# Performance work log

Hardware: AMD Instinct MI355X
Metric: run time of the kernel (lower is better)

The kernel has to match this reference:

```python
import jax, jax.numpy as jnp
import numpy as np

N_NODES = 100000
N_EDGES = 500000
IN_DIM, HID, N_CLS = 128, 512, 40


def gcn_conv(x, W, b, src, dst, num_nodes):
    # PyG GCNConv: h = x W; add self-loops; norm = d^-1/2[src] * d^-1/2[dst];
    # out[dst] += norm * h[src]; out += bias
    h = x @ W  # [N, out_dim]
    ones = jnp.ones(src.shape[0], dtype=x.dtype)
    deg = jax.ops.segment_sum(ones, dst, num_segments=num_nodes)  # in-degree incl self-loops
    dinv = jnp.where(deg > 0, jax.lax.rsqrt(deg), 0.0)
    norm = dinv[src] * dinv[dst]  # [E]
    msgs = h[src] * norm[:, None]  # [E, out_dim] gather + scale
    out = jax.ops.segment_sum(msgs, dst, num_segments=num_nodes)
    return out + b


def setup_inputs() -> dict:
    key = jax.random.key(0)
    k1, k2, k3, k4, k5, k6 = jax.random.split(key, 6)
    x = jax.random.normal(k1, (N_NODES, IN_DIM), dtype=jnp.float32)
    edge_index = jax.random.randint(k2, (2, N_EDGES), 0, N_NODES, dtype=jnp.int32)
    # Glorot-ish params
    W1 = jax.random.normal(k3, (IN_DIM, HID), dtype=jnp.float32) * (1.0 / np.sqrt(IN_DIM))
    b1 = jnp.zeros((HID,), dtype=jnp.float32)
    W2 = jax.random.normal(k4, (HID, N_CLS), dtype=jnp.float32) * (1.0 / np.sqrt(HID))
    b2 = jnp.zeros((N_CLS,), dtype=jnp.float32)
    return {"x": x, "edge_index": edge_index, "W1": W1, "b1": b1, "W2": W2, "b2": b2}


def reference(x, edge_index, W1, b1, W2, b2):
    n = x.shape[0]
    # add self-loops once, shared by both conv layers
    loop = jnp.arange(n, dtype=edge_index.dtype)
    src = jnp.concatenate([edge_index[0], loop])
    dst = jnp.concatenate([edge_index[1], loop])
    h = gcn_conv(x, W1, b1, src, dst, n)
    h = jax.nn.relu(h)
    # dropout is identity in eval mode (reference computed in eval)
    h = gcn_conv(h, W2, b2, src, dst, n)
    return jax.nn.log_softmax(h, axis=1)
```

## Files before the change

kernel.cpp:

```cpp
#include <hip/hip_runtime.h>
#include <cstdint>
#include <cstddef>

#define N_NODES 100000
#define N_EDGES 500000
#define IN_DIM  128
#define HID     512
#define N_CLS   40
#define N_SBLK  ((N_NODES + 255) / 256)
#define N_CNTB  ((N_EDGES + 255) / 256)
#define N_XBFB  12500
#define N_PREPB 352

typedef short bf16x8 __attribute__((ext_vector_type(8)));
typedef float f32x4 __attribute__((ext_vector_type(4)));

__device__ inline unsigned short f2bf(float f) {
  unsigned u = __float_as_uint(f);
  u = u + 0x7fffu + ((u >> 16) & 1u);
  return (unsigned short)(u >> 16);
}
__device__ inline float blo(unsigned u) { return __uint_as_float(u << 16); }
__device__ inline float bhi(unsigned u) { return __uint_as_float(u & 0xffff0000u); }

__global__ __launch_bounds__(256) void k_zero(int* __restrict__ cnt, unsigned* __restrict__ flags) {
  int i = blockIdx.x * 256 + threadIdx.x;
  if (i < N_NODES) cnt[i] = 0;
  if (i < 512) flags[i] = 0;
}

__global__ __launch_bounds__(256) void k_count_xbf(const int* __restrict__ dst, int* __restrict__ cnt,
                                                   const float* __restrict__ x, uint2* __restrict__ xb2) {
  int b = blockIdx.x;
  if (b < N_CNTB) {
    int e = b * 256 + threadIdx.x;
    if (e < N_EDGES) atomicAdd(&cnt[dst[e]], 1);
  } else {
    int t = (b - N_CNTB) * 256 + threadIdx.x;
    float4 v = ((const float4*)x)[t];
    uint2 o;
    o.x = (unsigned)f2bf(v.x) | ((unsigned)f2bf(v.y) << 16);
    o.y = (unsigned)f2bf(v.z) | ((unsigned)f2bf(v.w) << 16);
    xb2[t] = o;
  }
}

__global__ __launch_bounds__(256) void k_scan_prep(const int* __restrict__ cnt, unsigned* __restrict__ flags,
                                                   int* __restrict__ offsets, int* __restrict__ cursor,
                                                   float* __restrict__ dinv,
                                                   const float* __restrict__ W1, const float* __restrict__ W2,
                                                   unsigned short* __restrict__ W1F, unsigned short* __restrict__ W2F) {
  int b = blockIdx.x;
  if (b < N_SBLK) {
    __shared__ int s[256];
    __shared__ int base_sh;
    int i = b * 256 + threadIdx.x;
    int v = (i < N_NODES) ? cnt[i] : 0;
    s[threadIdx.x] = v;
    __syncthreads();
    #pragma unroll
    for (int off = 1; off < 256; off <<= 1) {
      int t = (threadIdx.x >= off) ? s[threadIdx.x - off] : 0;
      __syncthreads();
      s[threadIdx.x] += t;
      __syncthreads();
    }
    int incl = s[threadIdx.x];
    if (threadIdx.x == 0) {
      int total = s[255];
      if (b == 0) {
        atomicExch(&flags[0], (2u << 30) | (unsigned)total);
        base_sh = 0;
      } else {
        atomicExch(&flags[b], (1u << 30) | (unsigned)total);
        int base = 0, pred = b - 1;
        while (true) {
          unsigned f;
          do { f = atomicAdd(&flags[pred], 0u); } while ((f >> 30) == 0u);
          base += (int)(f & 0x3fffffffu);
          if ((f >> 30) == 2u) break;
          --pred;
        }
        atomicExch(&flags[b], (2u << 30) | (unsigned)(base + (unsigned)total));
        base_sh = base;
      }
    }
    __syncthreads();
    int gbase = base_sh;
    if (i < N_NODES) {
      int excl = gbase + incl - v;
      offsets[i] = excl;
      cursor[i]  = excl;
      dinv[i]    = rsqrtf((float)(v + 1));
    }
    if (b == 0 && threadIdx.x == 0) offsets[N_NODES] = N_EDGES;
  } else {
    int t = (b - N_SBLK) * 256 + threadIdx.x;
    if (t < 65536) {
      int j = t & 7, lane = (t >> 3) & 63, rest = t >> 9;
      int s2 = rest & 3, c = rest >> 2;
      int k = s2 * 32 + (lane >> 4) * 8 + j;
      int n = c * 16 + (lane & 15);
      W1F[t] = f2bf(W1[k * HID + n]);
    } else {
      int u = t - 65536;
      int j = u & 7, lane = (u >> 3) & 63, rest = u >> 9;
      int ct = rest % 3, gk = rest / 3;
      int k = gk * 32 + (lane >> 4) * 8 + j;
      int col = ct * 16 + (lane & 15);
      W2F[u] = (col < N_CLS) ? f2bf(W2[k * N_CLS + col]) : (unsigned short)0;
    }
  }
}

__global__ __launch_bounds__(256) void k_fill(const int* __restrict__ src, const int* __restrict__ dst,
                                              const float* __restrict__ dinv,
                                              int* __restrict__ cursor, int2* __restrict__ epair) {
  int e = blockIdx.x * 256 + threadIdx.x;
  if (e >= N_EDGES) return;
  int s = src[e], d = dst[e];
  int pos = atomicAdd(&cursor[d], 1);
  float nrm = dinv[s] * dinv[d];
  epair[pos] = make_int2(s, __float_as_int(nrm));
}

__global__ __launch_bounds__(256) void k_gather1(const uint2* __restrict__ xb, const int2* __restrict__ ep,
                                                 const int* __restrict__ offsets,
                                                 const float* __restrict__ dinv, uint2* __restrict__ z1) {
  int lane = threadIdx.x & 63, h = lane >> 5, l = lane & 31;
  int d = blockIdx.x * 8 + (threadIdx.x >> 6) * 2 + h;
  int start = offsets[d], end = offsets[d + 1];
  float dd = dinv[d], sl = dd * dd;
  uint2 su = xb[(size_t)d * 32 + l];
  float a0 = sl * blo(su.x), a1 = sl * bhi(su.x), a2 = sl * blo(su.y), a3 = sl * bhi(su.y);
  float p0a = 0.f, p1a = 0.f, p2a = 0.f, p3a = 0.f;
  float q0a = 0.f, q1a = 0.f, q2a = 0.f, q3a = 0.f;
  float r0a = 0.f, r1a = 0.f, r2a = 0.f, r3a = 0.f;

  int i = start;
  for (; i + 3 < end; i += 4) {
    int2 e0 = ep[i], e1 = ep[i + 1], e2 = ep[i + 2], e3 = ep[i + 3];
    uint2 r0 = xb[(size_t)e0.x * 32 + l];
    uint2 r1 = xb[(size_t)e1.x * 32 + l];
    uint2 r2 = xb[(size_t)e2.x * 32 + l];
    uint2 r3 = xb[(size_t)e3.x * 32 + l];
    float n0 = __int_as_float(e0.y), n1 = __int_as_float(e1.y);
    float n2 = __int_as_float(e2.y), n3 = __int_as_float(e3.y);
    a0  += n0 * blo(r0.x); a1  += n0 * bhi(r0.x); a2  += n0 * blo(r0.y); a3  += n0 * bhi(r0.y);
    p0a += n1 * blo(r1.x); p1a += n1 * bhi(r1.x); p2a += n1 * blo(r1.y); p3a += n1 * bhi(r1.y);
    q0a += n2 * blo(r2.x); q1a += n2 * bhi(r2.x); q2a += n2 * blo(r2.y); q3a += n2 * bhi(r2.y);
    r0a += n3 * blo(r3.x); r1a += n3 * bhi(r3.x); r2a += n3 * blo(r3.y); r3a += n3 * bhi(r3.y);
  }
  for (; i < end; ++i) {
    int2 e0 = ep[i];
    uint2 r0 = xb[(size_t)e0.x * 32 + l];
    float n0 = __int_as_float(e0.y);
    a0 += n0 * blo(r0.x); a1 += n0 * bhi(r0.x); a2 += n0 * blo(r0.y); a3 += n0 * bhi(r0.y);
  }
  a0 += p0a + q0a + r0a;
  a1 += p1a + q1a + r1a;
  a2 += p2a + q2a + r2a;
  a3 += p3a + q3a + r3a;
  uint2 o;
  o.x = (unsigned)f2bf(a0) | ((unsigned)f2bf(a1) << 16);
  o.y = (unsigned)f2bf(a2) | ((unsigned)f2bf(a3) << 16);
  z1[(size_t)d * 32 + l] = o;
}

#define HS_STRIDE 56
__global__ __launch_bounds__(256) void k_fused_mfma(const unsigned short* __restrict__ z1b,
                                                    const unsigned short* __restrict__ W1F,
                                                    const float* __restrict__ b1,
                                                    const unsigned short* __restrict__ W2F,
                                                    unsigned short* __restrict__ Pb) {
  __shared__ unsigned short Hs[4][64 * HS_STRIDE];
  const int tid  = threadIdx.x;
  const int w    = tid >> 6, lane = tid & 63;
  const int c16  = lane & 15, quad = lane >> 4;
  const int mbase = blockIdx.x * 256 + w * 64;

  bf16x8 afrag[4][4];
  #pragma unroll
  for (int t = 0; t < 4; ++t) {
    int mrow = mbase + t * 16 + c16;
    int meff = (mrow < N_NODES) ? mrow : 0;
    const bf16x8* arow = (const bf16x8*)(z1b + (size_t)meff * IN_DIM + quad * 8);
    afrag[t][0] = arow[0];
    afrag[t][1] = arow[4];
    afrag[t][2] = arow[8];
    afrag[t][3] = arow[12];
  }

  f32x4 pacc[4][3];
  #pragma unroll
  for (int t = 0; t < 4; ++t)
    #pragma unroll
    for (int ct = 0; ct < 3; ++ct) pacc[t][ct] = (f32x4){0.f, 0.f, 0.f, 0.f};

  const bf16x8* w1f = (const bf16x8*)W1F;
  const bf16x8* w2f = (const bf16x8*)W2F;
  unsigned short* hs = Hs[w];

  for (int g = 0; g < 16; ++g) {
    #pragma unroll
    for (int nt = 0; nt < 2; ++nt) {
      int c = g * 2 + nt;
      bf16x8 bp0 = w1f[(c * 4 + 0) * 64 + lane];
      bf16x8 bp1 = w1f[(c * 4 + 1) * 64 + lane];
      bf16x8 bp2 = w1f[(c * 4 + 2) * 64 + lane];
      bf16x8 bp3 = w1f[(c * 4 + 3) * 64 + lane];
      f32x4 h[4];
      #pragma unroll
      for (int t = 0; t < 4; ++t) h[t] = (f32x4){0.f, 0.f, 0.f, 0.f};
      #pragma unroll
      for (int t = 0; t < 4; ++t) h[t] = __builtin_amdgcn_mfma_f32_16x16x32_bf16(afrag[t][0], bp0, h[t], 0, 0, 0);
      #pragma unroll
      for (int t = 0; t < 4; ++t) h[t] = __builtin_amdgcn_mfma_f32_16x16x32_bf16(afrag[t][1], bp1, h[t], 0, 0, 0);
      #pragma unroll
      for (int t = 0; t < 4; ++t) h[t] = __builtin_amdgcn_mfma_f32_16x16x32_bf16(afrag[t][2], bp2, h[t], 0, 0, 0);
      #pragma unroll
      for (int t = 0; t < 4; ++t) h[t] = __builtin_amdgcn_mfma_f32_16x16x32_bf16(afrag[t][3], bp3, h[t], 0, 0, 0);
      float bias = b1[c * 16 + c16];
      #pragma unroll
      for (int t = 0; t < 4; ++t)
        #pragma unroll
        for (int r = 0; r < 4; ++r)
          hs[(t * 16 + quad * 4 + r) * HS_STRIDE + nt * 16 + c16] = f2bf(fmaxf(h[t][r] + bias, 0.f));
    }
    bf16x8 hf[4];
    #pragma unroll
    for (int t = 0; t < 4; ++t)
      hf[t] = *(const bf16x8*)(hs + (t * 16 + c16) * HS_STRIDE + quad * 8);
    #pragma unroll
    for (int ct = 0; ct < 3; ++ct) {
      bf16x8 bf = w2f[(g * 3 + ct) * 64 + lane];
      #pragma unroll
      for (int t = 0; t < 4; ++t)
        pacc[t][ct] = __builtin_amdgcn_mfma_f32_16x16x32_bf16(hf[t], bf, pacc[t][ct], 0, 0, 0);
    }
  }

  #pragma unroll
  for (int t = 0; t < 4; ++t) {
    int mrow0 = mbase + t * 16 + quad * 4;
    #pragma unroll
    for (int ct = 0; ct < 3; ++ct) {
      int col = ct * 16 + c16;
      if (col < N_CLS) {
        #pragma unroll
        for (int r = 0; r < 4; ++r) {
          int m = mrow0 + r;
          if (m < N_NODES) Pb[(size_t)m * N_CLS + col] = f2bf(pacc[t][ct][r]);
        }
      }
    }
  }
}

__global__ __launch_bounds__(256) void k_gather2_lsm(const uint2* __restrict__ Pu2,
                                                     const int2* __restrict__ ep,
                                                     const int* __restrict__ offsets,
                                                     const float* __restrict__ dinv, const float* __restrict__ b2,
                                                     float* __restrict__ out) {
  int lane = threadIdx.x & 63, q = lane >> 4, l = lane & 15;
  int d = blockIdx.x * 16 + (threadIdx.x >> 6) * 4 + q;
  bool act = l < 10;
  int lc = act ? l : 0;
  int start = offsets[d], end = offsets[d + 1];
  float dd = dinv[d], sl = dd * dd;

  uint2 su = Pu2[(size_t)d * 10 + lc];
  float a0 = sl * blo(su.x), a1 = sl * bhi(su.x), a2 = sl * blo(su.y), a3 = sl * bhi(su.y);
  float p0a = 0.f, p1a = 0.f, p2a = 0.f, p3a = 0.f;
  float q0a = 0.f, q1a = 0.f, q2a = 0.f, q3a = 0.f;
  float r0a = 0.f, r1a = 0.f, r2a = 0.f, r3a = 0.f;

  int i = start;
  for (; i + 3 < end; i += 4) {
    int2 e0 = ep[i], e1 = ep[i + 1], e2 = ep[i + 2], e3 = ep[i + 3];
    uint2 u0 = Pu2[(size_t)e0.x * 10 + lc];
    uint2 u1 = Pu2[(size_t)e1.x * 10 + lc];
    uint2 u2 = Pu2[(size_t)e2.x * 10 + lc];
    uint2 u3 = Pu2[(size_t)e3.x * 10 + lc];
    float n0 = __int_as_float(e0.y), n1 = __int_as_float(e1.y);
    float n2 = __int_as_float(e2.y), n3 = __int_as_float(e3.y);
    a0  += n0 * blo(u0.x); a1  += n0 * bhi(u0.x); a2  += n0 * blo(u0.y); a3  += n0 * bhi(u0.y);
    p0a += n1 * blo(u1.x); p1a += n1 * bhi(u1.x); p2a += n1 * blo(u1.y); p3a += n1 * bhi(u1.y);
    q0a += n2 * blo(u2.x); q1a += n2 * bhi(u2.x); q2a += n2 * blo(u2.y); q3a += n2 * bhi(u2.y);
    r0a += n3 * blo(u3.x); r1a += n3 * bhi(u3.x); r2a += n3 * blo(u3.y); r3a += n3 * bhi(u3.y);
  }
  for (; i < end; ++i) {
    int2 e0 = ep[i];
    uint2 u0 = Pu2[(size_t)e0.x * 10 + lc];
    float n0 = __int_as_float(e0.y);
    a0 += n0 * blo(u0.x); a1 += n0 * bhi(u0.x); a2 += n0 * blo(u0.y); a3 += n0 * bhi(u0.y);
  }

  float v0, v1, v2, v3;
  if (act) {
    float4 bb = ((const float4*)b2)[l];
    v0 = a0 + p0a + q0a + r0a + bb.x;
    v1 = a1 + p1a + q1a + r1a + bb.y;
    v2 = a2 + p2a + q2a + r2a + bb.z;
    v3 = a3 + p3a + q3a + r3a + bb.w;
  } else {
    v0 = v1 = v2 = v3 = -1e30f;
  }
  float m = fmaxf(fmaxf(v0, v1), fmaxf(v2, v3));
  #pragma unroll
  for (int off = 8; off > 0; off >>= 1) m = fmaxf(m, __shfl_xor(m, off, 64));
  float e = act ? (expf(v0 - m) + expf(v1 - m) + expf(v2 - m) + expf(v3 - m)) : 0.f;
  float s = e;
  #pragma unroll
  for (int off = 8; off > 0; off >>= 1) s += __shfl_xor(s, off, 64);
  float lse = m + logf(s);
  if (act) {
    float4 o = make_float4(v0 - lse, v1 - lse, v2 - lse, v3 - lse);
    ((float4*)(out + (size_t)d * N_CLS))[l] = o;
  }
}

extern "C" void kernel_launch(void* const* d_in, const int* in_sizes, int n_in,
                              void* d_out, int out_size, void* d_ws, size_t ws_size,
                              hipStream_t stream) {
  const float* x  = (const float*)d_in[0];
  const int*   ei = (const int*)d_in[1];
  const int*  src = ei;
  const int*  dst = ei + N_EDGES;
  const float* W1 = (const float*)d_in[2];
  const float* b1 = (const float*)d_in[3];
  const float* W2 = (const float*)d_in[4];
  const float* b2 = (const float*)d_in[5];
  float* out = (float*)d_out;

  float* dinv    = (float*)d_ws;
  int*   cnt     = (int*)(dinv + 131072);
  int*   offsets = cnt + 131072;
  int*   cursor  = offsets + 131072;
  unsigned* flags = (unsigned*)(cursor + 131072);
  int2*  epair   = (int2*)(flags + 1024);
  uint2* xb2     = (uint2*)(epair + 524288);
  unsigned short* Pb = (unsigned short*)xb2;
  unsigned short* z1b = (unsigned short*)(xb2 + 3200000);
  unsigned short* W1F = z1b + (size_t)N_NODES * IN_DIM;
  unsigned short* W2F = W1F + HID * IN_DIM;

  k_zero <<<(N_NODES + 255) / 256, 256, 0, stream>>>(cnt, flags);
  k_count_xbf<<<N_CNTB + N_XBFB, 256, 0, stream>>>(dst, cnt, x, xb2);
  k_scan_prep<<<N_SBLK + N_PREPB, 256, 0, stream>>>(cnt, flags, offsets, cursor, dinv, W1, W2, W1F, W2F);
  k_fill <<<N_CNTB, 256, 0, stream>>>(src, dst, dinv, cursor, epair);
  k_gather1<<<N_NODES / 8, 256, 0, stream>>>(xb2, epair, offsets, dinv, (uint2*)z1b);
  k_fused_mfma<<<(N_NODES + 255) / 256, 256, 0, stream>>>(z1b, W1F, b1, W2F, Pb);
  k_gather2_lsm<<<N_NODES / 16, 256, 0, stream>>>((const uint2*)Pb, epair, offsets, dinv, b2, out);
}
```

Baseline: 247.4 us.

## Use nontemporal loads/stores, predicated 8-wide gather loops, and memset zeroing

Replaces the custom zero kernel with two hipMemsetAsync calls. Adds nontemporal stores for the bf16 x copy, z1, P and the final output, and nontemporal loads for the edge pairs. Rewrites both gather loops as 8-wide predicated batches, with invalid slots clamped to index 0 and weight 0, and two accumulator sets instead of four plus a tail loop. This aims to keep more gathers in flight and reduce cache pollution from streaming data. In exchange it issues wasted loads for short neighbor lists and reads epair past end, and nontemporal stores of data that is read back soon may lose cache reuse.

```diff
diff --git a/kernel.cpp b/kernel.cpp
--- a/kernel.cpp
+++ b/kernel.cpp
@@ -14,6 +14,8 @@
 
 typedef short bf16x8 __attribute__((ext_vector_type(8)));
 typedef float f32x4 __attribute__((ext_vector_type(4)));
+typedef int   i32x2 __attribute__((ext_vector_type(2)));
+typedef unsigned u32x2 __attribute__((ext_vector_type(2)));
 
 __device__ inline unsigned short f2bf(float f) {
   unsigned u = __float_as_uint(f);
@@ -23,14 +25,8 @@
 __device__ inline float blo(unsigned u) { return __uint_as_float(u << 16); }
 __device__ inline float bhi(unsigned u) { return __uint_as_float(u & 0xffff0000u); }
 
-__global__ __launch_bounds__(256) void k_zero(int* __restrict__ cnt, unsigned* __restrict__ flags) {
-  int i = blockIdx.x * 256 + threadIdx.x;
-  if (i < N_NODES) cnt[i] = 0;
-  if (i < 512) flags[i] = 0;
-}
-
 __global__ __launch_bounds__(256) void k_count_xbf(const int* __restrict__ dst, int* __restrict__ cnt,
-                                                   const float* __restrict__ x, uint2* __restrict__ xb2) {
+                                                   const float* __restrict__ x, unsigned* __restrict__ xb) {
   int b = blockIdx.x;
   if (b < N_CNTB) {
     int e = b * 256 + threadIdx.x;
@@ -38,10 +34,10 @@
   } else {
     int t = (b - N_CNTB) * 256 + threadIdx.x;
     float4 v = ((const float4*)x)[t];
-    uint2 o;
+    u32x2 o;
     o.x = (unsigned)f2bf(v.x) | ((unsigned)f2bf(v.y) << 16);
     o.y = (unsigned)f2bf(v.z) | ((unsigned)f2bf(v.w) << 16);
-    xb2[t] = o;
+    __builtin_nontemporal_store(o, (u32x2*)(xb + 2 * (size_t)t));
   }
 }
 
@@ -124,47 +120,35 @@
   epair[pos] = make_int2(s, __float_as_int(nrm));
 }
 
-__global__ __launch_bounds__(256) void k_gather1(const uint2* __restrict__ xb, const int2* __restrict__ ep,
+__global__ __launch_bounds__(256) void k_gather1(const uint2* __restrict__ xb, const i32x2* __restrict__ ep,
                                                  const int* __restrict__ offsets,
-                                                 const float* __restrict__ dinv, uint2* __restrict__ z1) {
+                                                 const float* __restrict__ dinv, unsigned* __restrict__ z1) {
   int lane = threadIdx.x & 63, h = lane >> 5, l = lane & 31;
   int d = blockIdx.x * 8 + (threadIdx.x >> 6) * 2 + h;
   int start = offsets[d], end = offsets[d + 1];
   float dd = dinv[d], sl = dd * dd;
   uint2 su = xb[(size_t)d * 32 + l];
-  float a0 = sl * blo(su.x), a1 = sl * bhi(su.x), a2 = sl * blo(su.y), a3 = sl * bhi(su.y);
-  float p0a = 0.f, p1a = 0.f, p2a = 0.f, p3a = 0.f;
-  float q0a = 0.f, q1a = 0.f, q2a = 0.f, q3a = 0.f;
-  float r0a = 0.f, r1a = 0.f, r2a = 0.f, r3a = 0.f;
-
-  int i = start;
-  for (; i + 3 < end; i += 4) {
-    int2 e0 = ep[i], e1 = ep[i + 1], e2 = ep[i + 2], e3 = ep[i + 3];
-    uint2 r0 = xb[(size_t)e0.x * 32 + l];
-    uint2 r1 = xb[(size_t)e1.x * 32 + l];
-    uint2 r2 = xb[(size_t)e2.x * 32 + l];
-    uint2 r3 = xb[(size_t)e3.x * 32 + l];
-    float n0 = __int_as_float(e0.y), n1 = __int_as_float(e1.y);
-    float n2 = __int_as_float(e2.y), n3 = __int_as_float(e3.y);
-    a0  += n0 * blo(r0.x); a1  += n0 * bhi(r0.x); a2  += n0 * blo(r0.y); a3  += n0 * bhi(r0.y);
-    p0a += n1 * blo(r1.x); p1a += n1 * bhi(r1.x); p2a += n1 * blo(r1.y); p3a += n1 * bhi(r1.y);
-    q0a += n2 * blo(r2.x); q1a += n2 * bhi(r2.x); q2a += n2 * blo(r2.y); q3a += n2 * bhi(r2.y);
-    r0a += n3 * blo(r3.x); r1a += n3 * bhi(r3.x); r2a += n3 * blo(r3.y); r3a += n3 * bhi(r3.y);
-  }
-  for (; i < end; ++i) {
-    int2 e0 = ep[i];
-    uint2 r0 = xb[(size_t)e0.x * 32 + l];
-    float n0 = __int_as_float(e0.y);
-    a0 += n0 * blo(r0.x); a1 += n0 * bhi(r0.x); a2 += n0 * blo(r0.y); a3 += n0 * bhi(r0.y);
-  }
-  a0 += p0a + q0a + r0a;
-  a1 += p1a + q1a + r1a;
-  a2 += p2a + q2a + r2a;
-  a3 += p3a + q3a + r3a;
-  uint2 o;
-  o.x = (unsigned)f2bf(a0) | ((unsigned)f2bf(a1) << 16);
-  o.y = (unsigned)f2bf(a2) | ((unsigned)f2bf(a3) << 16);
-  z1[(size_t)d * 32 + l] = o;
+  float s0 = sl * blo(su.x), s1 = sl * bhi(su.x), s2 = sl * blo(su.y), s3 = sl * bhi(su.y);
+  float t0 = 0.f, t1 = 0.f, t2 = 0.f, t3 = 0.f;
+
+  for (int i = start; i < end; i += 8) {
+    i32x2 e[8];
+    #pragma unroll
+    for (int k = 0; k < 8; ++k) e[k] = __builtin_nontemporal_load(&ep[i + k]);
+    #pragma unroll
+    for (int k = 0; k < 8; ++k) {
+      bool val = (i + k) < end;
+      int idx  = val ? e[k].x : 0;
+      float n  = val ? __int_as_float(e[k].y) : 0.f;
+      uint2 r  = xb[(size_t)idx * 32 + l];
+      if (k & 1) { t0 += n * blo(r.x); t1 += n * bhi(r.x); t2 += n * blo(r.y); t3 += n * bhi(r.y); }
+      else       { s0 += n * blo(r.x); s1 += n * bhi(r.x); s2 += n * blo(r.y); s3 += n * bhi(r.y); }
+    }
+  }
+  u32x2 o;
+  o.x = (unsigned)f2bf(s0 + t0) | ((unsigned)f2bf(s1 + t1) << 16);
+  o.y = (unsigned)f2bf(s2 + t2) | ((unsigned)f2bf(s3 + t3) << 16);
+  __builtin_nontemporal_store(o, (u32x2*)(z1 + 2 * ((size_t)d * 32 + l)));
 }
 
 #define HS_STRIDE 56
@@ -250,7 +234,8 @@
         #pragma unroll
         for (int r = 0; r < 4; ++r) {
           int m = mrow0 + r;
-          if (m < N_NODES) Pb[(size_t)m * N_CLS + col] = f2bf(pacc[t][ct][r]);
+          if (m < N_NODES)
+            __builtin_nontemporal_store(f2bf(pacc[t][ct][r]), &Pb[(size_t)m * N_CLS + col]);
         }
       }
     }
@@ -258,7 +243,7 @@
 }
 
 __global__ __launch_bounds__(256) void k_gather2_lsm(const uint2* __restrict__ Pu2,
-                                                     const int2* __restrict__ ep,
+                                                     const i32x2* __restrict__ ep,
                                                      const int* __restrict__ offsets,
                                                      const float* __restrict__ dinv, const float* __restrict__ b2,
                                                      float* __restrict__ out) {
@@ -270,39 +255,31 @@
   float dd = dinv[d], sl = dd * dd;
 
   uint2 su = Pu2[(size_t)d * 10 + lc];
-  float a0 = sl * blo(su.x), a1 = sl * bhi(su.x), a2 = sl * blo(su.y), a3 = sl * bhi(su.y);
-  float p0a = 0.f, p1a = 0.f, p2a = 0.f, p3a = 0.f;
-  float q0a = 0.f, q1a = 0.f, q2a = 0.f, q3a = 0.f;
-  float r0a = 0.f, r1a = 0.f, r2a = 0.f, r3a = 0.f;
-
-  int i = start;
-  for (; i + 3 < end; i += 4) {
-    int2 e0 = ep[i], e1 = ep[i + 1], e2 = ep[i + 2], e3 = ep[i + 3];
-    uint2 u0 = Pu2[(size_t)e0.x * 10 + lc];
-    uint2 u1 = Pu2[(size_t)e1.x * 10 + lc];
-    uint2 u2 = Pu2[(size_t)e2.x * 10 + lc];
-    uint2 u3 = Pu2[(size_t)e3.x * 10 + lc];
-    float n0 = __int_as_float(e0.y), n1 = __int_as_float(e1.y);
-    float n2 = __int_as_float(e2.y), n3 = __int_as_float(e3.y);
-    a0  += n0 * blo(u0.x); a1  += n0 * bhi(u0.x); a2  += n0 * blo(u0.y); a3  += n0 * bhi(u0.y);
-    p0a += n1 * blo(u1.x); p1a += n1 * bhi(u1.x); p2a += n1 * blo(u1.y); p3a += n1 * bhi(u1.y);
-    q0a += n2 * blo(u2.x); q1a += n2 * bhi(u2.x); q2a += n2 * blo(u2.y); q3a += n2 * bhi(u2.y);
-    r0a += n3 * blo(u3.x); r1a += n3 * bhi(u3.x); r2a += n3 * blo(u3.y); r3a += n3 * bhi(u3.y);
-  }
-  for (; i < end; ++i) {
-    int2 e0 = ep[i];
-    uint2 u0 = Pu2[(size_t)e0.x * 10 + lc];
-    float n0 = __int_as_float(e0.y);
-    a0 += n0 * blo(u0.x); a1 += n0 * bhi(u0.x); a2 += n0 * blo(u0.y); a3 += n0 * bhi(u0.y);
+  float s0 = sl * blo(su.x), s1 = sl * bhi(su.x), s2 = sl * blo(su.y), s3 = sl * bhi(su.y);
+  float t0 = 0.f, t1 = 0.f, t2 = 0.f, t3 = 0.f;
+
+  for (int i = start; i < end; i += 8) {
+    i32x2 e[8];
+    #pragma unroll
+    for (int k = 0; k < 8; ++k) e[k] = __builtin_nontemporal_load(&ep[i + k]);
+    #pragma unroll
+    for (int k = 0; k < 8; ++k) {
+      bool val = (i + k) < end;
+      int idx  = val ? e[k].x : 0;
+      float n  = val ? __int_as_float(e[k].y) : 0.f;
+      uint2 u  = Pu2[(size_t)idx * 10 + lc];
+      if (k & 1) { t0 += n * blo(u.x); t1 += n * bhi(u.x); t2 += n * blo(u.y); t3 += n * bhi(u.y); }
+      else       { s0 += n * blo(u.x); s1 += n * bhi(u.x); s2 += n * blo(u.y); s3 += n * bhi(u.y); }
+    }
   }
 
   float v0, v1, v2, v3;
   if (act) {
     float4 bb = ((const float4*)b2)[l];
-    v0 = a0 + p0a + q0a + r0a + bb.x;
-    v1 = a1 + p1a + q1a + r1a + bb.y;
-    v2 = a2 + p2a + q2a + r2a + bb.z;
-    v3 = a3 + p3a + q3a + r3a + bb.w;
+    v0 = s0 + t0 + bb.x;
+    v1 = s1 + t1 + bb.y;
+    v2 = s2 + t2 + bb.z;
+    v3 = s3 + t3 + bb.w;
   } else {
     v0 = v1 = v2 = v3 = -1e30f;
   }
@@ -315,8 +292,8 @@
   for (int off = 8; off > 0; off >>= 1) s += __shfl_xor(s, off, 64);
   float lse = m + logf(s);
   if (act) {
-    float4 o = make_float4(v0 - lse, v1 - lse, v2 - lse, v3 - lse);
-    ((float4*)(out + (size_t)d * N_CLS))[l] = o;
+    f32x4 o = (f32x4){v0 - lse, v1 - lse, v2 - lse, v3 - lse};
+    __builtin_nontemporal_store(o, (f32x4*)(out + (size_t)d * N_CLS + 4 * l));
   }
 }
 
@@ -345,11 +322,12 @@
   unsigned short* W1F = z1b + (size_t)N_NODES * IN_DIM;
   unsigned short* W2F = W1F + HID * IN_DIM;
 
-  k_zero <<<(N_NODES + 255) / 256, 256, 0, stream>>>(cnt, flags);
-  k_count_xbf<<<N_CNTB + N_XBFB, 256, 0, stream>>>(dst, cnt, x, xb2);
+  (void)hipMemsetAsync(cnt, 0, N_NODES * sizeof(int), stream);
+  (void)hipMemsetAsync(flags, 0, 512 * sizeof(unsigned), stream);
+  k_count_xbf<<<N_CNTB + N_XBFB, 256, 0, stream>>>(dst, cnt, x, (unsigned*)xb2);
   k_scan_prep<<<N_SBLK + N_PREPB, 256, 0, stream>>>(cnt, flags, offsets, cursor, dinv, W1, W2, W1F, W2F);
   k_fill <<<N_CNTB, 256, 0, stream>>>(src, dst, dinv, cursor, epair);
-  k_gather1<<<N_NODES / 8, 256, 0, stream>>>(xb2, epair, offsets, dinv, (uint2*)z1b);
+  k_gather1<<<N_NODES / 8, 256, 0, stream>>>(xb2, (const i32x2*)epair, offsets, dinv, (unsigned*)z1b);
   k_fused_mfma<<<(N_NODES + 255) / 256, 256, 0, stream>>>(z1b, W1F, b1, W2F, Pb);
-  k_gather2_lsm<<<N_NODES / 16, 256, 0, stream>>>((const uint2*)Pb, epair, offsets, dinv, b2, out);
-}
+  k_gather2_lsm<<<N_NODES / 16, 256, 0, stream>>>((const uint2*)Pb, (const i32x2*)epair, offsets, dinv, b2, out);
+}
```

New measurement: 252.6 us. 2.1% more time.
